# Kernel tuning notes

Hardware: AMD Instinct MI355X
Metric: run time of the kernel (lower is better)

The kernel has to match this reference:

```python
import jax, jax.numpy as jnp
import numpy as np

N_NODES = 50000
N_EDGES = 1600000
D_IN = 128
D_HID = 128
D_OUT = 128


def setup_inputs() -> dict:
    key = jax.random.key(0)
    k1, k2, k3, k4, k5, k6 = jax.random.split(key, 6)
    x = jax.random.normal(k1, (N_NODES, D_IN), dtype=jnp.float32)
    edge_index = jax.random.randint(k2, (2, N_EDGES), 0, N_NODES, dtype=jnp.int64)
    # glorot-ish init for GCNConv linear weights; bias zeros-like but randomized small
    W1 = jax.random.normal(k3, (D_IN, D_HID), dtype=jnp.float32) * (1.0 / np.sqrt(D_IN))
    b1 = jax.random.normal(k4, (D_HID,), dtype=jnp.float32) * 0.01
    W2 = jax.random.normal(k5, (D_HID, D_OUT), dtype=jnp.float32) * (1.0 / np.sqrt(D_HID))
    b2 = jax.random.normal(k6, (D_OUT,), dtype=jnp.float32) * 0.01
    return {"x": x, "edge_index": edge_index, "W1": W1, "b1": b1, "W2": W2, "b2": b2}


def gcn_conv(x, src, dst, W, b, n_nodes):
    # PyG GCNConv: add self-loops, symmetric normalization deg^-1/2, lin -> aggregate -> +bias
    loop = jnp.arange(n_nodes, dtype=src.dtype)
    s = jnp.concatenate([src, loop])  # [E+N]
    d = jnp.concatenate([dst, loop])  # [E+N]
    deg = jax.ops.segment_sum(jnp.ones_like(d, dtype=x.dtype), d, num_segments=n_nodes)
    dinv = jnp.where(deg > 0, jax.lax.rsqrt(deg), 0.0)
    norm = dinv[s] * dinv[d]  # [E+N]
    h = x @ W  # [N, F_out]
    msg = h[s] * norm[:, None]  # gather + scale: [E+N, F_out]
    out = jax.ops.segment_sum(msg, d, num_segments=n_nodes)  # scatter-add
    return out + b


def reference(x, edge_index, W1, b1, W2, b2):
    src, dst = edge_index[0], edge_index[1]
    h = gcn_conv(x, src, dst, W1, b1, N_NODES)
    h = jnp.where(h >= 0, h, 0.1 * h)  # LeakyReLU(0.1)
    h = gcn_conv(h, src, dst, W2, b2, N_NODES)
    return h.mean(axis=1)  # [N]
```

## Files before the change

kernel.cpp:

```cpp
#include <hip/hip_runtime.h>
#include <hip/hip_bf16.h>


#define N_NODES 50000
#define NPAD 50048
#define D 128
#define BK 196
#define CHUNK 4096

typedef unsigned int uint;
typedef unsigned short u16;
typedef __attribute__((ext_vector_type(8))) short short8;
typedef __attribute__((ext_vector_type(4))) float floatx4;

__device__ __forceinline__ u16 cvt_bf16(float f) {
    uint u = __float_as_uint(f);
    return (u16)((u + 0x7fffu + ((u >> 16) & 1u)) >> 16);
}
__device__ __forceinline__ uint pack_bf2(float a, float b) {
    return (uint)cvt_bf16(a) | ((uint)cvt_bf16(b) << 16);
}

__global__ void hist_w2m_kernel(const int* __restrict__ dst, uint* __restrict__ H,
                                const float* __restrict__ W2, const float* __restrict__ b2,
                                float* __restrict__ w2m, uint* __restrict__ counter,
                                int E, int CHN) {
    int t = threadIdx.x, c = blockIdx.x;
    if (c < CHN) {
        __shared__ uint h[BK];
        if (t < BK) h[t] = 0;
        __syncthreads();
        int e0 = c * CHUNK;
        for (int i = t; i < CHUNK; i += 256) {
            int e = e0 + i;
            if (e < E) atomicAdd(&h[dst[e] >> 8], 1u);
        }
        __syncthreads();
        if (t < BK) H[t * CHN + c] = h[t];
    } else {
        int wave = t >> 6, lane = t & 63;
        int k = (c - CHN) * 4 + wave;
        if (k < 128) {
            float s = W2[k * 128 + lane] + W2[k * 128 + 64 + lane];
#pragma unroll
            for (int off = 32; off > 0; off >>= 1) s += __shfl_down(s, off, 64);
            if (lane == 0) w2m[k] = s * (1.0f / 128.0f);
        } else if (k == 128) {
            float s = b2[lane] + b2[lane + 64];
#pragma unroll
            for (int off = 32; off > 0; off >>= 1) s += __shfl_down(s, off, 64);
            if (lane == 0) w2m[128] = s * (1.0f / 128.0f);
        } else if (k == 129) {
            if (lane == 0) *counter = 0;
        }
    }
}

__global__ void scan_kernel(uint* __restrict__ H, uint* __restrict__ T, uint* __restrict__ B,
                            int* __restrict__ row, uint* __restrict__ counter,
                            int CHN, int E, int N) {
    __shared__ uint s[256];
    __shared__ uint ticket_sh;
    int t = threadIdx.x, b = blockIdx.x;
    uint carry = 0;
    for (int base = 0; base < CHN; base += 256) {
        int idx = base + t;
        uint v = (idx < CHN) ? H[b * CHN + idx] : 0u;
        s[t] = v;
        __syncthreads();
#pragma unroll
        for (int off = 1; off < 256; off <<= 1) {
            uint u = (t >= off) ? s[t - off] : 0u;
            __syncthreads();
            s[t] += u;
            __syncthreads();
        }
        if (idx < CHN) H[b * CHN + idx] = carry + s[t] - v;
        carry += s[255];
        __syncthreads();
    }
    if (t == 0) {
        atomicExch(&T[b], carry);
        __threadfence();
        ticket_sh = atomicAdd(counter, 1);
    }
    __syncthreads();
    if (ticket_sh == (uint)(gridDim.x - 1)) {
        __threadfence();
        uint v = (t < BK) ? atomicAdd(&T[t], 0u) : 0u;
        s[t] = v;
        __syncthreads();
#pragma unroll
        for (int off = 1; off < 256; off <<= 1) {
            uint u = (t >= off) ? s[t - off] : 0u;
            __syncthreads();
            s[t] += u;
            __syncthreads();
        }
        if (t < BK) B[t] = s[t] - v;
        if (t == 0) { B[BK] = (uint)E; row[N] = E; }
    }
}

__global__ void scatter_kernel(const int* __restrict__ src, const int* __restrict__ dst,
                               const uint* __restrict__ H, const uint* __restrict__ B,
                               uint* __restrict__ EB, int E, int CHN) {
    __shared__ uint cur[BK];
    int t = threadIdx.x, c = blockIdx.x;
    if (t < BK) cur[t] = B[t] + H[t * CHN + c];
    __syncthreads();
    int e0 = c * CHUNK;
    for (int i = t; i < CHUNK; i += 256) {
        int e = e0 + i;
        if (e < E) {
            int d = dst[e];
            uint slot = atomicAdd(&cur[d >> 8], 1u);
            EB[slot] = ((uint)(d & 255) << 16) | (uint)src[e];
        }
    }
}

#define WT_STRIDE 136
union SortGemmSmem {
    struct { uint cnt[256], s[256], cur[256]; } sort;
    u16 wt[128 * WT_STRIDE];
};
__global__ __launch_bounds__(256) void sortgemm_kernel(
    const uint* __restrict__ EB, const uint* __restrict__ B,
    int* __restrict__ row, float* __restrict__ dinv, u16* __restrict__ esrc,
    const float* __restrict__ A, const float* __restrict__ W,
    uint* __restrict__ G32, int N, int M) {
    __shared__ SortGemmSmem sm;
    int t = threadIdx.x;

    if (blockIdx.x < BK) {
        int b = blockIdx.x;
        uint base = B[b], ne = B[b + 1] - base;
        sm.sort.cnt[t] = 0;
        __syncthreads();
        for (uint i = t; i < ne; i += 256) atomicAdd(&sm.sort.cnt[EB[base + i] >> 16], 1u);
        __syncthreads();
        uint c = sm.sort.cnt[t];
        sm.sort.s[t] = c;
        __syncthreads();
#pragma unroll
        for (int off = 1; off < 256; off <<= 1) {
            uint u = (t >= off) ? sm.sort.s[t - off] : 0u;
            __syncthreads();
            sm.sort.s[t] += u;
            __syncthreads();
        }
        uint p = sm.sort.s[t] - c;
        int v = (b << 8) + t;
        if (v < N) {
            row[v] = (int)(base + p);
            dinv[v] = rsqrtf((float)(c + 1u));
        }
        sm.sort.cur[t] = base + p;
        __syncthreads();
        for (uint i = t; i < ne; i += 256) {
            uint u = EB[base + i];
            uint slot = atomicAdd(&sm.sort.cur[u >> 16], 1u);
            esrc[slot] = (u16)(u & 0xffffu);
        }
    } else {
        int bid = blockIdx.x - BK;
        for (int i = t; i < 128 * 128; i += 256) {
            int k = i >> 7, n = i & 127;
            sm.wt[n * WT_STRIDE + k] = cvt_bf16(W[i]);
        }
        __syncthreads();

        int wave = t >> 6, lane = t & 63;
        int m = lane & 15, quad = lane >> 4;
        int rowa = bid * 64 + wave * 16 + m;
        int rowc = rowa < M ? rowa : M - 1;
        const float* Arow = A + (long)rowc * D;

        short8 afrag[4];
#pragma unroll
        for (int kt = 0; kt < 4; kt++) {
            int k0 = kt * 32 + quad * 8;
            float4 f0 = *(const float4*)(Arow + k0);
            float4 f1 = *(const float4*)(Arow + k0 + 4);
            short8 af;
            af[0] = (short)cvt_bf16(f0.x); af[1] = (short)cvt_bf16(f0.y);
            af[2] = (short)cvt_bf16(f0.z); af[3] = (short)cvt_bf16(f0.w);
            af[4] = (short)cvt_bf16(f1.x); af[5] = (short)cvt_bf16(f1.y);
            af[6] = (short)cvt_bf16(f1.z); af[7] = (short)cvt_bf16(f1.w);
            afrag[kt] = af;
        }

        int orow0 = bid * 64 + wave * 16;
        for (int n0 = 0; n0 < 128; n0 += 16) {
            floatx4 acc = {0.f, 0.f, 0.f, 0.f};
#pragma unroll
            for (int kt = 0; kt < 4; kt++) {
                short8 bf = *(const short8*)(sm.wt + (n0 + m) * WT_STRIDE + kt * 32 + quad * 8);
                acc = __builtin_amdgcn_mfma_f32_16x16x32_bf16(afrag[kt], bf, acc, 0, 0, 0);
            }
#pragma unroll
            for (int r = 0; r < 4; r++) {
                float val = acc[r];
                float oth = __shfl_xor(val, 1, 64);
                int orow = orow0 + quad * 4 + r;
                if (orow < M && (m & 1) == 0)
                    G32[(long)orow * 64 + ((n0 + m) >> 1)] = pack_bf2(val, oth);
            }
        }
    }
}

__global__ __launch_bounds__(256) void gather_node_kernel(
    const int* __restrict__ row, const u16* __restrict__ esrc,
    const uint* __restrict__ g16, const float* __restrict__ dinv,
    const float* __restrict__ b1, const float* __restrict__ w2m,
    float* __restrict__ mg, int N) {
    int wave = threadIdx.x >> 6;
    int lane = threadIdx.x & 63;
    int sub = lane & 7;
    int nb = lane >> 3;
    int v = blockIdx.x * 4 + wave;
    if (v >= N) return;

    const uint4* gv = (const uint4*)g16;
    float dvv = dinv[v];
    float acc[16];
#pragma unroll
    for (int i = 0; i < 16; i++) acc[i] = 0.f;

#define ACC8(ua, ub, wgt) {                                              \
    uint uu[8] = {(ua).x, (ua).y, (ua).z, (ua).w, (ub).x, (ub).y, (ub).z, (ub).w}; \
    _Pragma("unroll")                                                    \
    for (int i = 0; i < 8; i++) {                                        \
        acc[2*i]   += (wgt) * __uint_as_float(uu[i] << 16);              \
        acc[2*i+1] += (wgt) * __uint_as_float(uu[i] & 0xffff0000u);      \
    } }

    if (nb == 0) {
        long rb = (long)v * 16 + 2 * sub;
        uint4 ua = gv[rb], ub = gv[rb + 1];
        ACC8(ua, ub, dvv)
    }
    int jb = row[v], je = row[v + 1];
    int j = jb + nb;
    if (j < je) {
        int s0 = esrc[j];
        float wA = dinv[s0];
        long r0 = (long)s0 * 16 + 2 * sub;
        uint4 p0 = gv[r0], p1 = gv[r0 + 1];
        j += 8;
        while (j < je) {
            int s1 = esrc[j];
            float wB = dinv[s1];
            long r1 = (long)s1 * 16 + 2 * sub;
            uint4 q0 = gv[r1], q1 = gv[r1 + 1];
            j += 8;
            ACC8(p0, p1, wA)
            p0 = q0; p1 = q1; wA = wB;
        }
        ACC8(p0, p1, wA)
    }
#undef ACC8

#pragma unroll
    for (int i = 0; i < 16; i++) {
        acc[i] += __shfl_xor(acc[i], 8, 64);
        acc[i] += __shfl_xor(acc[i], 16, 64);
        acc[i] += __shfl_xor(acc[i], 32, 64);
    }

    if (nb == 0) {
        const float4* bp = (const float4*)b1;
        const float4* wp = (const float4*)w2m;
        float s = 0.f;
#pragma unroll
        for (int q4 = 0; q4 < 4; q4++) {
            float4 bb = bp[sub * 4 + q4];
            float4 wm = wp[sub * 4 + q4];
            float t0 = dvv * acc[4*q4 + 0] + bb.x; t0 = t0 >= 0.f ? t0 : 0.1f * t0;
            float t1 = dvv * acc[4*q4 + 1] + bb.y; t1 = t1 >= 0.f ? t1 : 0.1f * t1;
            float t2 = dvv * acc[4*q4 + 2] + bb.z; t2 = t2 >= 0.f ? t2 : 0.1f * t2;
            float t3 = dvv * acc[4*q4 + 3] + bb.w; t3 = t3 >= 0.f ? t3 : 0.1f * t3;
            s += t0 * wm.x + t1 * wm.y + t2 * wm.z + t3 * wm.w;
        }
        s += __shfl_xor(s, 1, 64);
        s += __shfl_xor(s, 2, 64);
        s += __shfl_xor(s, 4, 64);
        if (sub == 0) mg[v] = dvv * s;
    }
}

__global__ void out_kernel(const int* __restrict__ row, const u16* __restrict__ esrc,
                           const float* __restrict__ mg, const float* __restrict__ dinv,
                           const float* __restrict__ w2m, float* __restrict__ out, int N) {
    int v = blockIdx.x * blockDim.x + threadIdx.x;
    if (v >= N) return;
    float acc = mg[v];
    int jb = row[v], je = row[v + 1];
    int j = jb;
    for (; j + 8 <= je; j += 8) {
        acc += mg[esrc[j]] + mg[esrc[j + 1]] + mg[esrc[j + 2]] + mg[esrc[j + 3]] +
               mg[esrc[j + 4]] + mg[esrc[j + 5]] + mg[esrc[j + 6]] + mg[esrc[j + 7]];
    }
    for (; j < je; j++) acc += mg[esrc[j]];
    out[v] = dinv[v] * acc + w2m[128];
}

extern "C" void kernel_launch(void* const* d_in, const int* in_sizes, int n_in,
                              void* d_out, int out_size, void* d_ws, size_t ws_size,
                              hipStream_t stream) {
    const float* x  = (const float*)d_in[0];
    const int* ei   = (const int*)d_in[1];
    const float* W1 = (const float*)d_in[2];
    const float* b1 = (const float*)d_in[3];
    const float* W2 = (const float*)d_in[4];
    const float* b2 = (const float*)d_in[5];
    float* out = (float*)d_out;

    const int N = N_NODES;
    const int E = in_sizes[1] / 2;
    const int* src = ei;
    const int* dst = ei + E;
    const int CHN = (E + CHUNK - 1) / CHUNK;
    const int nblocks = (N + 255) / 256;

    float*    dinv    = (float*)d_ws;
    int*      row     = (int*)(dinv + NPAD);
    uint*     B       = (uint*)(row + NPAD + 16);
    float*    w2m     = (float*)(B + 256);
    float*    mg      = w2m + 256;
    uint*     T       = (uint*)(mg + NPAD);
    uint*     counter = T + 256;
    uint*     g16u    = counter + 16;
    u16*      esrc    = (u16*)(g16u + (long)NPAD * 64);
    uint*     H       = (uint*)(esrc + E);
    uint*     EB      = H + BK * CHN;

    hist_w2m_kernel<<<CHN + 33, 256, 0, stream>>>(dst, H, W2, b2, w2m, counter, E, CHN);
    scan_kernel<<<BK, 256, 0, stream>>>(H, T, B, row, counter, CHN, E, N);
    scatter_kernel<<<CHN, 256, 0, stream>>>(src, dst, H, B, EB, E, CHN);
    sortgemm_kernel<<<BK + (N + 63) / 64, 256, 0, stream>>>(EB, B, row, dinv, esrc,
                                                            x, W1, g16u, N, N);
    gather_node_kernel<<<(N + 3) / 4, 256, 0, stream>>>(row, esrc, g16u, dinv, b1, w2m, mg, N);
    out_kernel<<<nblocks, 256, 0, stream>>>(row, esrc, mg, dinv, w2m, out, N);
}
```

Baseline: 197.9 us.

## Fuse histogram, scan, scatter, sort and GEMM into one persistent kernel with grid barriers

Merges the four graph-build kernels (histogram, bucket scan, scatter, per-bucket sort) plus the X·W1 GEMM and the W2 mean reduction into a single launch. Stages are ordered with global atomic tick counters and spin-wait barriers, and the counters are reset by a memset. This removes kernel-launch gaps and lets the independent GEMM blocks overlap the sort phases. It relies on all CHN (391) build blocks being co-resident to avoid deadlock, and adds spin-wait overhead.

```diff
diff --git a/kernel.cpp b/kernel.cpp
--- a/kernel.cpp
+++ b/kernel.cpp
@@ -8,6 +8,11 @@
 #define BK 196
 #define CHUNK 4096
 
+#define TICK_H 0
+#define TICK_S 1
+#define TICK_B 2
+#define TICK_X 3
+
 typedef unsigned int uint;
 typedef unsigned short u16;
 typedef __attribute__((ext_vector_type(8))) short short8;
@@ -21,150 +26,149 @@
     return (uint)cvt_bf16(a) | ((uint)cvt_bf16(b) << 16);
 }
 
-__global__ void hist_w2m_kernel(const int* __restrict__ dst, uint* __restrict__ H,
-                                const float* __restrict__ W2, const float* __restrict__ b2,
-                                float* __restrict__ w2m, uint* __restrict__ counter,
-                                int E, int CHN) {
-    int t = threadIdx.x, c = blockIdx.x;
-    if (c < CHN) {
-        __shared__ uint h[BK];
-        if (t < BK) h[t] = 0;
-        __syncthreads();
-        int e0 = c * CHUNK;
-        for (int i = t; i < CHUNK; i += 256) {
-            int e = e0 + i;
-            if (e < E) atomicAdd(&h[dst[e] >> 8], 1u);
-        }
-        __syncthreads();
-        if (t < BK) H[t * CHN + c] = h[t];
-    } else {
-        int wave = t >> 6, lane = t & 63;
-        int k = (c - CHN) * 4 + wave;
-        if (k < 128) {
-            float s = W2[k * 128 + lane] + W2[k * 128 + 64 + lane];
-#pragma unroll
-            for (int off = 32; off > 0; off >>= 1) s += __shfl_down(s, off, 64);
-            if (lane == 0) w2m[k] = s * (1.0f / 128.0f);
-        } else if (k == 128) {
-            float s = b2[lane] + b2[lane + 64];
-#pragma unroll
-            for (int off = 32; off > 0; off >>= 1) s += __shfl_down(s, off, 64);
-            if (lane == 0) w2m[128] = s * (1.0f / 128.0f);
-        } else if (k == 129) {
-            if (lane == 0) *counter = 0;
-        }
-    }
-}
-
-__global__ void scan_kernel(uint* __restrict__ H, uint* __restrict__ T, uint* __restrict__ B,
-                            int* __restrict__ row, uint* __restrict__ counter,
-                            int CHN, int E, int N) {
-    __shared__ uint s[256];
-    __shared__ uint ticket_sh;
-    int t = threadIdx.x, b = blockIdx.x;
-    uint carry = 0;
-    for (int base = 0; base < CHN; base += 256) {
-        int idx = base + t;
-        uint v = (idx < CHN) ? H[b * CHN + idx] : 0u;
-        s[t] = v;
-        __syncthreads();
-#pragma unroll
-        for (int off = 1; off < 256; off <<= 1) {
-            uint u = (t >= off) ? s[t - off] : 0u;
-            __syncthreads();
-            s[t] += u;
-            __syncthreads();
-        }
-        if (idx < CHN) H[b * CHN + idx] = carry + s[t] - v;
-        carry += s[255];
-        __syncthreads();
-    }
-    if (t == 0) {
-        atomicExch(&T[b], carry);
-        __threadfence();
-        ticket_sh = atomicAdd(counter, 1);
-    }
+__device__ __forceinline__ void bar_arrive(uint* flag) {
     __syncthreads();
-    if (ticket_sh == (uint)(gridDim.x - 1)) {
-        __threadfence();
-        uint v = (t < BK) ? atomicAdd(&T[t], 0u) : 0u;
-        s[t] = v;
-        __syncthreads();
-#pragma unroll
-        for (int off = 1; off < 256; off <<= 1) {
-            uint u = (t >= off) ? s[t - off] : 0u;
-            __syncthreads();
-            s[t] += u;
-            __syncthreads();
-        }
-        if (t < BK) B[t] = s[t] - v;
-        if (t == 0) { B[BK] = (uint)E; row[N] = E; }
-    }
-}
-
-__global__ void scatter_kernel(const int* __restrict__ src, const int* __restrict__ dst,
-                               const uint* __restrict__ H, const uint* __restrict__ B,
-                               uint* __restrict__ EB, int E, int CHN) {
-    __shared__ uint cur[BK];
-    int t = threadIdx.x, c = blockIdx.x;
-    if (t < BK) cur[t] = B[t] + H[t * CHN + c];
+    __threadfence();
+    if (threadIdx.x == 0) atomicAdd(flag, 1u);
+}
+__device__ __forceinline__ void bar_wait(uint* flag, uint target) {
+    if (threadIdx.x == 0) {
+        while (atomicAdd(flag, 0u) < target) __builtin_amdgcn_s_sleep(2);
+    }
     __syncthreads();
-    int e0 = c * CHUNK;
-    for (int i = t; i < CHUNK; i += 256) {
-        int e = e0 + i;
-        if (e < E) {
-            int d = dst[e];
-            uint slot = atomicAdd(&cur[d >> 8], 1u);
-            EB[slot] = ((uint)(d & 255) << 16) | (uint)src[e];
-        }
-    }
+    __threadfence();
 }
 
 #define WT_STRIDE 136
-union SortGemmSmem {
+union BuildSmem {
+    uint h[256];
+    uint s[256];
+    uint cur[256];
     struct { uint cnt[256], s[256], cur[256]; } sort;
     u16 wt[128 * WT_STRIDE];
 };
-__global__ __launch_bounds__(256) void sortgemm_kernel(
-    const uint* __restrict__ EB, const uint* __restrict__ B,
+
+__global__ __launch_bounds__(256) void build_kernel(
+    const int* __restrict__ src, const int* __restrict__ dst,
+    const float* __restrict__ A, const float* __restrict__ W,
+    const float* __restrict__ W2, const float* __restrict__ b2,
+    uint* __restrict__ H, uint* __restrict__ T, uint* __restrict__ B,
     int* __restrict__ row, float* __restrict__ dinv, u16* __restrict__ esrc,
-    const float* __restrict__ A, const float* __restrict__ W,
-    uint* __restrict__ G32, int N, int M) {
-    __shared__ SortGemmSmem sm;
+    uint* __restrict__ EB, uint* __restrict__ G32, float* __restrict__ w2m,
+    uint* __restrict__ tick, int E, int N, int CHN) {
+    __shared__ BuildSmem sm;
+    __shared__ uint tk_sh;
     int t = threadIdx.x;
-
-    if (blockIdx.x < BK) {
-        int b = blockIdx.x;
-        uint base = B[b], ne = B[b + 1] - base;
-        sm.sort.cnt[t] = 0;
+    int b = blockIdx.x;
+
+    if (b < CHN) {
+        if (t < BK) sm.h[t] = 0;
         __syncthreads();
-        for (uint i = t; i < ne; i += 256) atomicAdd(&sm.sort.cnt[EB[base + i] >> 16], 1u);
+        {
+            int e0 = b * CHUNK;
+            for (int i = t; i < CHUNK; i += 256) {
+                int e = e0 + i;
+                if (e < E) atomicAdd(&sm.h[dst[e] >> 8], 1u);
+            }
+        }
         __syncthreads();
-        uint c = sm.sort.cnt[t];
-        sm.sort.s[t] = c;
+        if (t < BK) H[t * CHN + b] = sm.h[t];
+        bar_arrive(&tick[TICK_H]);
+
+        if (b < BK) {
+            bar_wait(&tick[TICK_H], (uint)CHN);
+            uint carry = 0;
+            for (int base = 0; base < CHN; base += 256) {
+                int idx = base + t;
+                uint v = (idx < CHN) ? H[b * CHN + idx] : 0u;
+                sm.s[t] = v;
+                __syncthreads();
+#pragma unroll
+                for (int off = 1; off < 256; off <<= 1) {
+                    uint u = (t >= off) ? sm.s[t - off] : 0u;
+                    __syncthreads();
+                    sm.s[t] += u;
+                    __syncthreads();
+                }
+                if (idx < CHN) H[b * CHN + idx] = carry + sm.s[t] - v;
+                carry += sm.s[255];
+                __syncthreads();
+            }
+            if (t == 0) atomicExch(&T[b], carry);
+            __syncthreads();
+            __threadfence();
+            if (t == 0) tk_sh = atomicAdd(&tick[TICK_S], 1u);
+            __syncthreads();
+            if (tk_sh == BK - 1) {
+                __threadfence();
+                uint v = (t < BK) ? atomicAdd(&T[t], 0u) : 0u;
+                sm.s[t] = v;
+                __syncthreads();
+#pragma unroll
+                for (int off = 1; off < 256; off <<= 1) {
+                    uint u = (t >= off) ? sm.s[t - off] : 0u;
+                    __syncthreads();
+                    sm.s[t] += u;
+                    __syncthreads();
+                }
+                if (t < BK) B[t] = sm.s[t] - v;
+                if (t == 0) { B[BK] = (uint)E; row[N] = E; }
+                __syncthreads();
+                __threadfence();
+                if (t == 0) atomicExch(&tick[TICK_B], 1u);
+            }
+        }
+
+        bar_wait(&tick[TICK_B], 1u);
+        if (t < BK) sm.cur[t] = B[t] + H[t * CHN + b];
         __syncthreads();
-#pragma unroll
-        for (int off = 1; off < 256; off <<= 1) {
-            uint u = (t >= off) ? sm.sort.s[t - off] : 0u;
-            __syncthreads();
-            sm.sort.s[t] += u;
-            __syncthreads();
-        }
-        uint p = sm.sort.s[t] - c;
-        int v = (b << 8) + t;
-        if (v < N) {
-            row[v] = (int)(base + p);
-            dinv[v] = rsqrtf((float)(c + 1u));
-        }
-        sm.sort.cur[t] = base + p;
-        __syncthreads();
-        for (uint i = t; i < ne; i += 256) {
-            uint u = EB[base + i];
-            uint slot = atomicAdd(&sm.sort.cur[u >> 16], 1u);
-            esrc[slot] = (u16)(u & 0xffffu);
-        }
-    } else {
-        int bid = blockIdx.x - BK;
+        {
+            int e0 = b * CHUNK;
+            for (int i = t; i < CHUNK; i += 256) {
+                int e = e0 + i;
+                if (e < E) {
+                    int d = dst[e];
+                    uint slot = atomicAdd(&sm.cur[d >> 8], 1u);
+                    EB[slot] = ((uint)(d & 255) << 16) | (uint)src[e];
+                }
+            }
+        }
+        bar_arrive(&tick[TICK_X]);
+
+        if (b < BK) {
+            bar_wait(&tick[TICK_X], (uint)CHN);
+            uint base = B[b], ne = B[b + 1] - base;
+            sm.sort.cnt[t] = 0;
+            __syncthreads();
+            for (uint i = t; i < ne; i += 256) atomicAdd(&sm.sort.cnt[EB[base + i] >> 16], 1u);
+            __syncthreads();
+            uint c = sm.sort.cnt[t];
+            sm.sort.s[t] = c;
+            __syncthreads();
+#pragma unroll
+            for (int off = 1; off < 256; off <<= 1) {
+                uint u = (t >= off) ? sm.sort.s[t - off] : 0u;
+                __syncthreads();
+                sm.sort.s[t] += u;
+                __syncthreads();
+            }
+            uint p = sm.sort.s[t] - c;
+            int v = (b << 8) + t;
+            if (v < N) {
+                row[v] = (int)(base + p);
+                dinv[v] = rsqrtf((float)(c + 1u));
+            }
+            sm.sort.cur[t] = base + p;
+            __syncthreads();
+            for (uint i = t; i < ne; i += 256) {
+                uint u = EB[base + i];
+                uint slot = atomicAdd(&sm.sort.cur[u >> 16], 1u);
+                esrc[slot] = (u16)(u & 0xffffu);
+            }
+        }
+    } else if (b < CHN + (N + 63) / 64) {
+        int bid = b - CHN;
+        int M = N;
         for (int i = t; i < 128 * 128; i += 256) {
             int k = i >> 7, n = i & 127;
             sm.wt[n * WT_STRIDE + k] = cvt_bf16(W[i]);
@@ -207,6 +211,20 @@
                 if (orow < M && (m & 1) == 0)
                     G32[(long)orow * 64 + ((n0 + m) >> 1)] = pack_bf2(val, oth);
             }
+        }
+    } else {
+        int wave = t >> 6, lane = t & 63;
+        int k = (b - CHN - (N + 63) / 64) * 4 + wave;
+        if (k < 128) {
+            float s = W2[k * 128 + lane] + W2[k * 128 + 64 + lane];
+#pragma unroll
+            for (int off = 32; off > 0; off >>= 1) s += __shfl_down(s, off, 64);
+            if (lane == 0) w2m[k] = s * (1.0f / 128.0f);
+        } else if (k == 128) {
+            float s = b2[lane] + b2[lane + 64];
+#pragma unroll
+            for (int off = 32; off > 0; off >>= 1) s += __shfl_down(s, off, 64);
+            if (lane == 0) w2m[128] = s * (1.0f / 128.0f);
         }
     }
 }
@@ -325,23 +343,26 @@
     const int CHN = (E + CHUNK - 1) / CHUNK;
     const int nblocks = (N + 255) / 256;
 
-    float*    dinv    = (float*)d_ws;
+    uint*     tick    = (uint*)d_ws;
+    float*    dinv    = (float*)(tick + 16);
     int*      row     = (int*)(dinv + NPAD);
     uint*     B       = (uint*)(row + NPAD + 16);
     float*    w2m     = (float*)(B + 256);
     float*    mg      = w2m + 256;
     uint*     T       = (uint*)(mg + NPAD);
-    uint*     counter = T + 256;
-    uint*     g16u    = counter + 16;
+    uint*     g16u    = T + 256;
     u16*      esrc    = (u16*)(g16u + (long)NPAD * 64);
     uint*     H       = (uint*)(esrc + E);
     uint*     EB      = H + BK * CHN;
 
-    hist_w2m_kernel<<<CHN + 33, 256, 0, stream>>>(dst, H, W2, b2, w2m, counter, E, CHN);
-    scan_kernel<<<BK, 256, 0, stream>>>(H, T, B, row, counter, CHN, E, N);
-    scatter_kernel<<<CHN, 256, 0, stream>>>(src, dst, H, B, EB, E, CHN);
-    sortgemm_kernel<<<BK + (N + 63) / 64, 256, 0, stream>>>(EB, B, row, dinv, esrc,
-                                                            x, W1, g16u, N, N);
+    hipMemsetAsync(tick, 0, 64, stream);
+
+    const int gemm_blocks = (N + 63) / 64;
+    build_kernel<<<CHN + gemm_blocks + 33, 256, 0, stream>>>(
+        src, dst, x, W1, W2, b2, H, T, B, row, dinv, esrc, EB, g16u, w2m,
+        tick, E, N, CHN);
+
     gather_node_kernel<<<(N + 3) / 4, 256, 0, stream>>>(row, esrc, g16u, dinv, b1, w2m, mg, N);
+
     out_kernel<<<nblocks, 256, 0, stream>>>(row, esrc, mg, dinv, w2m, out, N);
 }
```

Measured after the change: 423.2 us. +113.8%, slower.
